# Kernel optimization log

Measured on AMD Instinct MI355X. Metric: run time of the kernel, lower is better.

## Reference

```python
import jax, jax.numpy as jnp
import numpy as np

B, T, I, H, E = 256, 128, 512, 1024, 256


def setup_inputs() -> dict:
    key = jax.random.key(0)
    ks = jax.random.split(key, 14)
    s = lambda *d: 1.0 / np.sqrt(d[-1])
    inp = {
        "x": jax.random.normal(ks[0], (B, T, I), jnp.float32),
        # encoder LSTMCell(I, H): weights [4H, *], gate order i,f,g,o (torch)
        "enc_Wih": jax.random.uniform(ks[1], (4 * H, I), jnp.float32, -s(H), s(H)),
        "enc_Whh": jax.random.uniform(ks[2], (4 * H, H), jnp.float32, -s(H), s(H)),
        "enc_bih": jax.random.uniform(ks[3], (4 * H,), jnp.float32, -s(H), s(H)),
        "enc_bhh": jax.random.uniform(ks[4], (4 * H,), jnp.float32, -s(H), s(H)),
        # enc_fc: H -> E
        "encfc_W": jax.random.uniform(ks[5], (E, H), jnp.float32, -s(H), s(H)),
        "encfc_b": jax.random.uniform(ks[6], (E,), jnp.float32, -s(H), s(H)),
        # dec_fc: E -> H
        "decfc_W": jax.random.uniform(ks[7], (H, E), jnp.float32, -s(E), s(E)),
        "decfc_b": jax.random.uniform(ks[8], (H,), jnp.float32, -s(E), s(E)),
        # decoder LSTMCell(H + I, I)
        "dec_Wih": jax.random.uniform(ks[9], (4 * I, H + I), jnp.float32, -s(I), s(I)),
        "dec_Whh": jax.random.uniform(ks[10], (4 * I, I), jnp.float32, -s(I), s(I)),
        "dec_bih": jax.random.uniform(ks[11], (4 * I,), jnp.float32, -s(I), s(I)),
        "dec_bhh": jax.random.uniform(ks[12], (4 * I,), jnp.float32, -s(I), s(I)),
    }
    return inp


def _gates(pre):
    i, f, g, o = jnp.split(pre, 4, axis=-1)
    return jax.nn.sigmoid(i), jax.nn.sigmoid(f), jnp.tanh(g), jax.nn.sigmoid(o)


def reference(x, enc_Wih, enc_Whh, enc_bih, enc_bhh, encfc_W, encfc_b,
              decfc_W, decfc_b, dec_Wih, dec_Whh, dec_bih, dec_bhh):
    b = x.shape[0]
    # ---- encoder: precompute input projections for all timesteps ----
    x_proj = jnp.einsum('btd,gd->tbg', x, enc_Wih) + (enc_bih + enc_bhh)  # [T,B,4H]

    def enc_step(carry, xp):
        h, c = carry
        i, f, g, o = _gates(xp + h @ enc_Whh.T)
        c = f * c + i * g
        h = o * jnp.tanh(c)
        return (h, c), None

    h0 = jnp.zeros((b, H), x.dtype)
    c0 = jnp.zeros((b, H), x.dtype)
    (_, c_final), _ = jax.lax.scan(enc_step, (h0, c0), x_proj)

    # NB: original code names the returned (h, c) as (o_t_enc, h_t_enc), so
    # embd is computed from the final CELL state -- replicated faithfully.
    embd = jax.nn.relu(c_final @ encfc_W.T + encfc_b)                # [B,E]
    dec_first_hidden = jax.nn.relu(embd @ decfc_W.T + decfc_b)       # [B,H]

    # ---- decoder: input at each step is cat(dec_first_hidden, h_prev) ----
    # (eval path: teacher forcing disabled; dec states init to zeros)
    fixed = dec_first_hidden @ dec_Wih[:, :H].T + (dec_bih + dec_bhh)  # [B,4I]
    W_rec = dec_Wih[:, H:] + dec_Whh  # input second-half and hidden are both h_prev

    def dec_step(carry, _):
        h, c = carry
        i, f, g, o = _gates(fixed + h @ W_rec.T)
        c = f * c + i * g
        h = o * jnp.tanh(c)
        return (h, c), h

    hd0 = jnp.zeros((b, I), x.dtype)
    cd0 = jnp.zeros((b, I), x.dtype)
    _, hs = jax.lax.scan(dec_step, (hd0, cd0), None, length=x.shape[1])  # [T,B,I]
    outputs = jnp.transpose(hs[::-1], (1, 0, 2))  # reversed, [B,T,I]
    return outputs, embd
```

## Files before the change

### kernel.cpp

```cpp
#include <hip/hip_runtime.h>
#include <hip/hip_fp16.h>


#define B_ 256
#define T_ 128
#define I_ 512
#define H_ 1024
#define E_ 256

typedef _Float16 half8 __attribute__((ext_vector_type(8)));
typedef float floatx4 __attribute__((ext_vector_type(4)));

__device__ __forceinline__ float sigmoidf_(float x) { return 1.0f / (1.0f + __expf(-x)); }
__device__ __forceinline__ float tanhf_(float x) {
    x = fminf(fmaxf(x, -15.0f), 15.0f);
    float e = __expf(2.0f * x);
    return (e - 1.0f) / (e + 1.0f);
}

__device__ __forceinline__ half8 ldg_h8_sc1(const _Float16* p) {
    union { unsigned long long u[2]; half8 h; } v;
    const unsigned long long* q = (const unsigned long long*)p;
    v.u[0] = __hip_atomic_load(q,     __ATOMIC_RELAXED, __HIP_MEMORY_SCOPE_AGENT);
    v.u[1] = __hip_atomic_load(q + 1, __ATOMIC_RELAXED, __HIP_MEMORY_SCOPE_AGENT);
    return v.h;
}
__device__ __forceinline__ void stg_h2_sc1(_Float16* p, float a, float b) {
    union { _Float16 h[2]; unsigned int u; } v;
    v.h[0] = (_Float16)a; v.h[1] = (_Float16)b;
    __hip_atomic_store((unsigned int*)p, v.u, __ATOMIC_RELAXED, __HIP_MEMORY_SCOPE_AGENT);
}
__device__ __forceinline__ void wait_vm0() {
    asm volatile("s_waitcnt vmcnt(0)" ::: "memory");
}
__device__ __forceinline__ void poll_rg(int* flags, int rgbase, int lane, int target) {
    while (__hip_atomic_load(&flags[rgbase + lane], __ATOMIC_RELAXED, __HIP_MEMORY_SCOPE_AGENT) < target)
        __builtin_amdgcn_s_sleep(1);
    asm volatile("" ::: "memory");
}

__global__ void shuffle_x_kernel(const float* __restrict__ x, _Float16* __restrict__ xf) {
    const int gg   = blockIdx.x * 256 + threadIdx.x;
    const int tile = gg >> 6;
    const int lane = gg & 63;
    const int t  = tile >> 8;
    const int rt = (tile >> 4) & 15;
    const int kc = tile & 15;
    const int b  = rt * 16 + (lane & 15);
    const int j0 = kc * 32 + ((lane >> 4) << 3);
    const float* src = x + ((size_t)b * T_ + t) * I_ + j0;
    float4 f0 = *(const float4*)src;
    float4 f1 = *(const float4*)(src + 4);
    half8 h = { (_Float16)f0.x, (_Float16)f0.y, (_Float16)f0.z, (_Float16)f0.w,
                (_Float16)f1.x, (_Float16)f1.y, (_Float16)f1.z, (_Float16)f1.w };
    *(half8*)(xf + (size_t)tile * 512 + lane * 8) = h;
}

__global__ __launch_bounds__(256) void small_gemm_kernel(
    const float* __restrict__ A, int lda,
    const float* __restrict__ W, int ldw,
    const float* __restrict__ b1, const float* __restrict__ b2,
    float* __restrict__ out, int N, int K, int relu)
{
    __shared__ float sA2[32][33];
    __shared__ float sW2[32][33];
    int tid = threadIdx.x;
    int tx = tid & 15, ty = tid >> 4;
    int m0 = blockIdx.y * 32, n0 = blockIdx.x * 32;
    float acc[2][2] = {};
    for (int k0 = 0; k0 < K; k0 += 32) {
        __syncthreads();
#pragma unroll
        for (int i = 0; i < 4; ++i) {
            int e = tid + i * 256;
            int r = e >> 5, c = e & 31;
            sA2[r][c] = A[(size_t)(m0 + r) * lda + k0 + c];
            sW2[r][c] = W[(size_t)(n0 + r) * ldw + k0 + c];
        }
        __syncthreads();
#pragma unroll
        for (int k = 0; k < 32; ++k) {
            float a0 = sA2[ty * 2][k], a1 = sA2[ty * 2 + 1][k];
            float w0 = sW2[tx * 2][k], w1 = sW2[tx * 2 + 1][k];
            acc[0][0] += a0 * w0; acc[0][1] += a0 * w1;
            acc[1][0] += a1 * w0; acc[1][1] += a1 * w1;
        }
    }
#pragma unroll
    for (int i = 0; i < 2; ++i)
#pragma unroll
        for (int j = 0; j < 2; ++j) {
            int m = m0 + ty * 2 + i, n = n0 + tx * 2 + j;
            float v = acc[i][j] + b1[n] + (b2 ? b2[n] : 0.0f);
            if (relu) v = fmaxf(v, 0.0f);
            out[(size_t)m * N + n] = v;
        }
}

__global__ __launch_bounds__(256, 1) void enc_persist(
    const _Float16* __restrict__ xf,
    const float* __restrict__ Wih, const float* __restrict__ Whh,
    const float* __restrict__ bih, const float* __restrict__ bhh,
    _Float16* __restrict__ hbuf, float* __restrict__ c_out, int* __restrict__ flags)
{
    const int tid  = threadIdx.x;
    const int wave = tid >> 6, lane = tid & 63;
    const int q = lane >> 4, n15 = lane & 15;
    const int blk = blockIdx.x;
    const int rg = blk >> 6, cc = blk & 63;

    half8 bw[4][12];
#pragma unroll
    for (int g = 0; g < 4; ++g) {
        const int jc = g * H_ + cc * 16 + n15;
#pragma unroll
        for (int kc = 0; kc < 12; ++kc) {
            const int k = (4 * kc + wave) * 32 + q * 8;
            const float* src = (k < I_) ? (Wih + (size_t)jc * I_ + k)
                                        : (Whh + (size_t)jc * H_ + (k - I_));
            float4 f0 = *(const float4*)src;
            float4 f1 = *(const float4*)(src + 4);
            bw[g][kc] = half8{(_Float16)f0.x, (_Float16)f0.y, (_Float16)f0.z, (_Float16)f0.w,
                              (_Float16)f1.x, (_Float16)f1.y, (_Float16)f1.z, (_Float16)f1.w};
        }
    }

    const int hcp = tid & 7;
    const int rT  = tid >> 3;
    float breg[4][2];
#pragma unroll
    for (int g = 0; g < 4; ++g)
#pragma unroll
        for (int e = 0; e < 2; ++e) {
            const int j = g * H_ + cc * 16 + 2 * hcp + e;
            breg[g][e] = bih[j] + bhh[j];
        }
    float creg[2][2] = {{0.f, 0.f}, {0.f, 0.f}};

    __shared__ float preT[4][64][35];
    const size_t laneoff = (size_t)lane * 8;

    for (int s = 0; s < T_; ++s) {
        const _Float16* __restrict__ hcur = hbuf + (size_t)(s & 1) * 262144;
        _Float16* __restrict__ hnxt = hbuf + (size_t)((s + 1) & 1) * 262144;

        floatx4 acc[4][4];
#pragma unroll
        for (int m = 0; m < 4; ++m)
#pragma unroll
            for (int n = 0; n < 4; ++n) acc[m][n] = floatx4{0.f, 0.f, 0.f, 0.f};

        half8 X[4][4];
#pragma unroll
        for (int kc = 0; kc < 4; ++kc)
#pragma unroll
            for (int m = 0; m < 4; ++m)
                X[kc][m] = *(const half8*)(xf + (((size_t)s * 16 + rg * 4 + m) * 16
                                                + (4 * kc + wave)) * 512 + laneoff);
#pragma unroll
        for (int kc = 0; kc < 4; ++kc)
#pragma unroll
            for (int n = 0; n < 4; ++n)
#pragma unroll
                for (int m = 0; m < 4; ++m)
                    acc[m][n] = __builtin_amdgcn_mfma_f32_16x16x32_f16(
                        X[kc][m], bw[n][kc], acc[m][n], 0, 0, 0);

        poll_rg(flags, rg * 64, lane, s);

        half8 Hb[4][4];
#pragma unroll
        for (int kc = 4; kc < 8; ++kc)
#pragma unroll
            for (int m = 0; m < 4; ++m)
                Hb[kc - 4][m] = ldg_h8_sc1(hcur + ((size_t)(rg * 4 + m) * 32
                                                   + (4 * kc + wave - 16)) * 512 + laneoff);
#pragma unroll
        for (int kc = 4; kc < 12; ++kc) {
            const int sl = kc & 3;
#pragma unroll
            for (int n = 0; n < 4; ++n)
#pragma unroll
                for (int m = 0; m < 4; ++m)
                    acc[m][n] = __builtin_amdgcn_mfma_f32_16x16x32_f16(
                        Hb[sl][m], bw[n][kc], acc[m][n], 0, 0, 0);
            if (kc < 8) {
#pragma unroll
                for (int m = 0; m < 4; ++m)
                    Hb[sl][m] = ldg_h8_sc1(hcur + ((size_t)(rg * 4 + m) * 32
                                                   + (4 * (kc + 4) + wave - 16)) * 512 + laneoff);
            }
        }

#pragma unroll
        for (int p = 0; p < 2; ++p) {
            if (p) __syncthreads();
#pragma unroll
            for (int m = 0; m < 2; ++m)
#pragma unroll
                for (int n = 0; n < 4; ++n)
#pragma unroll
                    for (int r = 0; r < 4; ++r)
                        preT[wave][n * 16 + n15][m * 16 + q * 4 + r] = acc[p * 2 + m][n][r];
            __syncthreads();
            float pg[4][2];
#pragma unroll
            for (int g = 0; g < 4; ++g)
#pragma unroll
                for (int e = 0; e < 2; ++e) {
                    const int col = g * 16 + 2 * hcp + e;
                    pg[g][e] = preT[0][col][rT] + preT[1][col][rT]
                             + preT[2][col][rT] + preT[3][col][rT] + breg[g][e];
                }
            float hv[2];
#pragma unroll
            for (int e = 0; e < 2; ++e) {
                const float ig = sigmoidf_(pg[0][e]);
                const float fg = sigmoidf_(pg[1][e]);
                const float gg = tanhf_(pg[2][e]);
                const float og = sigmoidf_(pg[3][e]);
                const float c  = fg * creg[p][e] + ig * gg;
                creg[p][e] = c;
                hv[e] = og * tanhf_(c);
            }
            const int row = p * 32 + rT;
            const int j   = cc * 16 + 2 * hcp;
            const int kch = j >> 5, j5 = j & 31;
            const int lt  = (row & 15) | ((j5 >> 3) << 4);
            stg_h2_sc1(hnxt + ((size_t)(rg * 4 + (row >> 4)) * 32 + kch) * 512
                            + lt * 8 + (j5 & 7), hv[0], hv[1]);
        }

        wait_vm0();
        __syncthreads();
        if (tid == 0)
            __hip_atomic_store(&flags[blk], s + 1, __ATOMIC_RELAXED, __HIP_MEMORY_SCOPE_AGENT);
    }

#pragma unroll
    for (int p = 0; p < 2; ++p)
        *(float2*)(c_out + (size_t)(rg * 64 + p * 32 + rT) * H_ + cc * 16 + 2 * hcp)
            = float2{creg[p][0], creg[p][1]};
}

__global__ __launch_bounds__(256, 1) void dec_persist(
    const float* __restrict__ dWih, const float* __restrict__ dWhh,
    const float* __restrict__ fixedb,
    _Float16* __restrict__ hbuf, float* __restrict__ out, int* __restrict__ flags)
{
    const int tid  = threadIdx.x;
    const int wave = tid >> 6, lane = tid & 63;
    const int q = lane >> 4, n15 = lane & 15;
    const int blk = blockIdx.x;
    const int rg = blk >> 6, cc = blk & 63;

    half8 bw[2][4];
#pragma unroll
    for (int n = 0; n < 2; ++n) {
        const int jc = (n * 2 + (n15 >> 3)) * I_ + cc * 8 + (n15 & 7);
#pragma unroll
        for (int kc = 0; kc < 4; ++kc) {
            const int k = wave * 128 + kc * 32 + q * 8;
            const float* s0 = dWih + (size_t)jc * (H_ + I_) + H_ + k;
            const float* s1 = dWhh + (size_t)jc * I_ + k;
            float4 a0 = *(const float4*)s0, a1 = *(const float4*)(s0 + 4);
            float4 b0 = *(const float4*)s1, b1 = *(const float4*)(s1 + 4);
            bw[n][kc] = half8{(_Float16)(a0.x + b0.x), (_Float16)(a0.y + b0.y),
                              (_Float16)(a0.z + b0.z), (_Float16)(a0.w + b0.w),
                              (_Float16)(a1.x + b1.x), (_Float16)(a1.y + b1.y),
                              (_Float16)(a1.z + b1.z), (_Float16)(a1.w + b1.w)};
        }
    }

    const int hcp = tid & 3;
    const int rT  = tid >> 2;
    const int brow = rg * 64 + rT;
    float fx[4][2];
#pragma unroll
    for (int g = 0; g < 4; ++g)
#pragma unroll
        for (int e = 0; e < 2; ++e)
            fx[g][e] = fixedb[(size_t)brow * (4 * I_) + g * I_ + cc * 8 + 2 * hcp + e];
    float creg2[2] = {0.f, 0.f};

    __shared__ float preT[4][32][67];
    const size_t laneoff = (size_t)lane * 8;

    for (int s = 0; s < T_; ++s) {
        const _Float16* __restrict__ hcur = hbuf + (size_t)(s & 1) * 131072;
        _Float16* __restrict__ hnxt = hbuf + (size_t)((s + 1) & 1) * 131072;

        poll_rg(flags, rg * 64, lane, s);

        half8 Hb[4][4];
#pragma unroll
        for (int kc = 0; kc < 4; ++kc)
#pragma unroll
            for (int m = 0; m < 4; ++m)
                Hb[kc][m] = ldg_h8_sc1(hcur + ((size_t)(rg * 4 + m) * 16
                                               + (wave * 4 + kc)) * 512 + laneoff);
        floatx4 acc[4][2];
#pragma unroll
        for (int m = 0; m < 4; ++m)
#pragma unroll
            for (int n = 0; n < 2; ++n) acc[m][n] = floatx4{0.f, 0.f, 0.f, 0.f};
#pragma unroll
        for (int kc = 0; kc < 4; ++kc)
#pragma unroll
            for (int n = 0; n < 2; ++n)
#pragma unroll
                for (int m = 0; m < 4; ++m)
                    acc[m][n] = __builtin_amdgcn_mfma_f32_16x16x32_f16(
                        Hb[kc][m], bw[n][kc], acc[m][n], 0, 0, 0);

#pragma unroll
        for (int p = 0; p < 2; ++p) {
            if (p) __syncthreads();
#pragma unroll
            for (int m = 0; m < 2; ++m)
#pragma unroll
                for (int n = 0; n < 2; ++n)
#pragma unroll
                    for (int r = 0; r < 4; ++r)
                        preT[wave][n * 16 + n15][m * 16 + q * 4 + r] = acc[p * 2 + m][n][r];
            __syncthreads();
            if ((rT >> 5) == p) {
                const int rl = rT & 31;
                float pg[4][2];
#pragma unroll
                for (int g = 0; g < 4; ++g)
#pragma unroll
                    for (int e = 0; e < 2; ++e) {
                        const int col = (g >> 1) * 16 + (g & 1) * 8 + 2 * hcp + e;
                        pg[g][e] = preT[0][col][rl] + preT[1][col][rl]
                                 + preT[2][col][rl] + preT[3][col][rl] + fx[g][e];
                    }
                float hv[2];
#pragma unroll
                for (int e = 0; e < 2; ++e) {
                    const float ig = sigmoidf_(pg[0][e]);
                    const float fg = sigmoidf_(pg[1][e]);
                    const float gg = tanhf_(pg[2][e]);
                    const float og = sigmoidf_(pg[3][e]);
                    const float c  = fg * creg2[e] + ig * gg;
                    creg2[e] = c;
                    hv[e] = og * tanhf_(c);
                }
                *(float2*)(out + ((size_t)brow * T_ + (T_ - 1 - s)) * I_ + cc * 8 + 2 * hcp)
                    = float2{hv[0], hv[1]};
                const int j = cc * 8 + 2 * hcp;
                const int kch = j >> 5, j5 = j & 31;
                const int lt  = (rT & 15) | ((j5 >> 3) << 4);
                stg_h2_sc1(hnxt + ((size_t)(rg * 4 + (rT >> 4)) * 16 + kch) * 512
                                + lt * 8 + (j5 & 7), hv[0], hv[1]);
            }
        }

        wait_vm0();
        __syncthreads();
        if (tid == 0)
            __hip_atomic_store(&flags[blk], s + 1, __ATOMIC_RELAXED, __HIP_MEMORY_SCOPE_AGENT);
    }
}

extern "C" void kernel_launch(void* const* d_in, const int* in_sizes, int n_in,
                              void* d_out_v, int out_size, void* d_ws, size_t ws_size,
                              hipStream_t stream) {
    (void)in_sizes; (void)n_in; (void)out_size; (void)ws_size;
    const float* x    = (const float*)d_in[0];
    const float* eWih = (const float*)d_in[1];
    const float* eWhh = (const float*)d_in[2];
    const float* ebih = (const float*)d_in[3];
    const float* ebhh = (const float*)d_in[4];
    const float* efcW = (const float*)d_in[5];
    const float* efcb = (const float*)d_in[6];
    const float* dfcW = (const float*)d_in[7];
    const float* dfcb = (const float*)d_in[8];
    const float* dWih = (const float*)d_in[9];
    const float* dWhh = (const float*)d_in[10];
    const float* dbih = (const float*)d_in[11];
    const float* dbhh = (const float*)d_in[12];
    float* d_out = (float*)d_out_v;

    char* ws = (char*)d_ws;
    size_t off = 0;
    auto carve = [&](size_t bytes) {
        char* p = ws + off;
        off += (bytes + 255) & ~(size_t)255;
        return p;
    };
    _Float16* xf     = (_Float16*)carve((size_t)B_ * T_ * I_ * 2);
    _Float16* hbufE  = (_Float16*)carve((size_t)2 * 262144 * 2);
    _Float16* hbufD  = (_Float16*)carve((size_t)2 * 131072 * 2);
    float*    c_e    = (float*)carve((size_t)B_ * H_ * 4);
    float*    fixedb = (float*)carve((size_t)B_ * 4 * I_ * 4);
    float*    dec1   = (float*)carve((size_t)B_ * H_ * 4);
    int*      flagsE = (int*)carve(256 * 4);
    int*      flagsD = (int*)carve(256 * 4);

    hipMemsetAsync(flagsE, 0, 256 * 4, stream);
    hipMemsetAsync(flagsD, 0, 256 * 4, stream);
    hipMemsetAsync(hbufE, 0, (size_t)262144 * 2, stream);
    hipMemsetAsync(hbufD, 0, (size_t)131072 * 2, stream);

    shuffle_x_kernel<<<dim3(8192), 256, 0, stream>>>(x, xf);

    enc_persist<<<dim3(256), 256, 0, stream>>>(xf, eWih, eWhh, ebih, ebhh,
                                               hbufE, c_e, flagsE);

    float* embd = d_out + (size_t)B_ * T_ * I_;
    small_gemm_kernel<<<dim3(E_ / 32, B_ / 32), 256, 0, stream>>>(
        c_e, H_, efcW, H_, efcb, nullptr, embd, E_, H_, 1);
    small_gemm_kernel<<<dim3(H_ / 32, B_ / 32), 256, 0, stream>>>(
        embd, E_, dfcW, E_, dfcb, nullptr, dec1, H_, E_, 1);
    small_gemm_kernel<<<dim3(4 * I_ / 32, B_ / 32), 256, 0, stream>>>(
        dec1, H_, dWih, H_ + I_, dbih, dbhh, fixedb, 4 * I_, H_, 0);

    dec_persist<<<dim3(256), 256, 0, stream>>>(dWih, dWhh, fixedb,
                                               hbufD, d_out, flagsD);
}
```

Baseline: 1.851 ms.

## Replace flag-based step sync with sentinel-filled per-step hidden buffers

The encoder and decoder persistent kernels no longer publish per-block step flags or poll them before loading the previous hidden state. Each timestep now writes to its own slice of a buffer sized T+1 steps, pre-filled with a 0x7C sentinel pattern. Consumers spin until the loaded chunks contain no sentinel words. This removes the flag round trip and the vmcnt(0) drain before signalling, so the next step can start as soon as its data lands. The cost is a much larger workspace and large memsets per call, and it relies on the fp16 sentinel (two +inf halves per word) never occurring in real data. The old flag path is kept as a fallback when the workspace is too small.

```diff
diff --git a/kernel.cpp b/kernel.cpp
--- a/kernel.cpp
+++ b/kernel.cpp
@@ -8,6 +8,10 @@
 #define H_ 1024
 #define E_ 256
 
+#define ENC_STEP 262144
+#define DEC_STEP 131072
+#define SENT32 0x7C7C7C7Cu
+
 typedef _Float16 half8 __attribute__((ext_vector_type(8)));
 typedef float floatx4 __attribute__((ext_vector_type(4)));
 
@@ -18,12 +22,33 @@
     return (e - 1.0f) / (e + 1.0f);
 }
 
-__device__ __forceinline__ half8 ldg_h8_sc1(const _Float16* p) {
-    union { unsigned long long u[2]; half8 h; } v;
+union HU { unsigned long long u[2]; half8 h; };
+
+__device__ __forceinline__ void ld_chunk(const _Float16* p, HU& v) {
     const unsigned long long* q = (const unsigned long long*)p;
     v.u[0] = __hip_atomic_load(q,     __ATOMIC_RELAXED, __HIP_MEMORY_SCOPE_AGENT);
     v.u[1] = __hip_atomic_load(q + 1, __ATOMIC_RELAXED, __HIP_MEMORY_SCOPE_AGENT);
-    return v.h;
+}
+__device__ __forceinline__ int chunk_ok(const HU& v) {
+    unsigned a = (unsigned)v.u[0], b = (unsigned)(v.u[0] >> 32);
+    unsigned c = (unsigned)v.u[1], d = (unsigned)(v.u[1] >> 32);
+    return (int)((a != SENT32) & (b != SENT32) & (c != SENT32) & (d != SENT32));
+}
+template <int STRIDE>
+__device__ __forceinline__ void load_grp(const _Float16* base, HU v[4]) {
+#pragma unroll
+    for (int m = 0; m < 4; ++m) ld_chunk(base + (size_t)m * STRIDE, v[m]);
+}
+template <int STRIDE>
+__device__ __forceinline__ void fix_grp(const _Float16* base, HU v[4]) {
+    while (!(chunk_ok(v[0]) & chunk_ok(v[1]) & chunk_ok(v[2]) & chunk_ok(v[3]))) {
+        __builtin_amdgcn_s_sleep(1);
+        load_grp<STRIDE>(base, v);
+    }
+}
+
+__device__ __forceinline__ half8 ldg_h8_sc1(const _Float16* p) {
+    HU v; ld_chunk(p, v); return v.h;
 }
 __device__ __forceinline__ void stg_h2_sc1(_Float16* p, float a, float b) {
     union { _Float16 h[2]; unsigned int u; } v;
@@ -97,11 +122,11 @@
         }
 }
 
-__global__ __launch_bounds__(256, 1) void enc_persist(
+__global__ __launch_bounds__(256, 1) void enc_df(
     const _Float16* __restrict__ xf,
     const float* __restrict__ Wih, const float* __restrict__ Whh,
     const float* __restrict__ bih, const float* __restrict__ bhh,
-    _Float16* __restrict__ hbuf, float* __restrict__ c_out, int* __restrict__ flags)
+    _Float16* __restrict__ hbuf, float* __restrict__ c_out)
 {
     const int tid  = threadIdx.x;
     const int wave = tid >> 6, lane = tid & 63;
@@ -141,8 +166,8 @@
     const size_t laneoff = (size_t)lane * 8;
 
     for (int s = 0; s < T_; ++s) {
-        const _Float16* __restrict__ hcur = hbuf + (size_t)(s & 1) * 262144;
-        _Float16* __restrict__ hnxt = hbuf + (size_t)((s + 1) & 1) * 262144;
+        const _Float16* __restrict__ hcur = hbuf + (size_t)s * ENC_STEP;
+        _Float16* __restrict__ hnxt = hbuf + (size_t)(s + 1) * ENC_STEP;
 
         floatx4 acc[4][4];
 #pragma unroll
@@ -166,30 +191,25 @@
                     acc[m][n] = __builtin_amdgcn_mfma_f32_16x16x32_f16(
                         X[kc][m], bw[n][kc], acc[m][n], 0, 0, 0);
 
-        poll_rg(flags, rg * 64, lane, s);
-
-        half8 Hb[4][4];
+        HU Hb[4][4];
 #pragma unroll
         for (int kc = 4; kc < 8; ++kc)
-#pragma unroll
-            for (int m = 0; m < 4; ++m)
-                Hb[kc - 4][m] = ldg_h8_sc1(hcur + ((size_t)(rg * 4 + m) * 32
-                                                   + (4 * kc + wave - 16)) * 512 + laneoff);
+            load_grp<32 * 512>(hcur + ((size_t)(rg * 4) * 32 + (4 * kc + wave - 16)) * 512
+                                    + laneoff, Hb[kc - 4]);
 #pragma unroll
         for (int kc = 4; kc < 12; ++kc) {
             const int sl = kc & 3;
+            fix_grp<32 * 512>(hcur + ((size_t)(rg * 4) * 32 + (4 * kc + wave - 16)) * 512
+                                   + laneoff, Hb[sl]);
 #pragma unroll
             for (int n = 0; n < 4; ++n)
 #pragma unroll
                 for (int m = 0; m < 4; ++m)
                     acc[m][n] = __builtin_amdgcn_mfma_f32_16x16x32_f16(
-                        Hb[sl][m], bw[n][kc], acc[m][n], 0, 0, 0);
-            if (kc < 8) {
-#pragma unroll
-                for (int m = 0; m < 4; ++m)
-                    Hb[sl][m] = ldg_h8_sc1(hcur + ((size_t)(rg * 4 + m) * 32
-                                                   + (4 * (kc + 4) + wave - 16)) * 512 + laneoff);
-            }
+                        Hb[sl][m].h, bw[n][kc], acc[m][n], 0, 0, 0);
+            if (kc < 8)
+                load_grp<32 * 512>(hcur + ((size_t)(rg * 4) * 32 + (4 * (kc + 4) + wave - 16)) * 512
+                                        + laneoff, Hb[sl]);
         }
 
 #pragma unroll
@@ -230,11 +250,7 @@
             stg_h2_sc1(hnxt + ((size_t)(rg * 4 + (row >> 4)) * 32 + kch) * 512
                             + lt * 8 + (j5 & 7), hv[0], hv[1]);
         }
-
-        wait_vm0();
         __syncthreads();
-        if (tid == 0)
-            __hip_atomic_store(&flags[blk], s + 1, __ATOMIC_RELAXED, __HIP_MEMORY_SCOPE_AGENT);
     }
 
 #pragma unroll
@@ -243,10 +259,10 @@
             = float2{creg[p][0], creg[p][1]};
 }
 
-__global__ __launch_bounds__(256, 1) void dec_persist(
+__global__ __launch_bounds__(256, 1) void dec_df(
     const float* __restrict__ dWih, const float* __restrict__ dWhh,
     const float* __restrict__ fixedb,
-    _Float16* __restrict__ hbuf, float* __restrict__ out, int* __restrict__ flags)
+    _Float16* __restrict__ hbuf, float* __restrict__ out)
 {
     const int tid  = threadIdx.x;
     const int wave = tid >> 6, lane = tid & 63;
@@ -287,31 +303,31 @@
     const size_t laneoff = (size_t)lane * 8;
 
     for (int s = 0; s < T_; ++s) {
-        const _Float16* __restrict__ hcur = hbuf + (size_t)(s & 1) * 131072;
-        _Float16* __restrict__ hnxt = hbuf + (size_t)((s + 1) & 1) * 131072;
-
-        poll_rg(flags, rg * 64, lane, s);
-
-        half8 Hb[4][4];
+        const _Float16* __restrict__ hcur = hbuf + (size_t)s * DEC_STEP;
+        _Float16* __restrict__ hnxt = hbuf + (size_t)(s + 1) * DEC_STEP;
+
+        HU Hb[4][4];
 #pragma unroll
         for (int kc = 0; kc < 4; ++kc)
-#pragma unroll
-            for (int m = 0; m < 4; ++m)
-                Hb[kc][m] = ldg_h8_sc1(hcur + ((size_t)(rg * 4 + m) * 16
-                                               + (wave * 4 + kc)) * 512 + laneoff);
+            load_grp<16 * 512>(hcur + ((size_t)(rg * 4) * 16 + (wave * 4 + kc)) * 512
+                                    + laneoff, Hb[kc]);
+
         floatx4 acc[4][2];
 #pragma unroll
         for (int m = 0; m < 4; ++m)
 #pragma unroll
             for (int n = 0; n < 2; ++n) acc[m][n] = floatx4{0.f, 0.f, 0.f, 0.f};
 #pragma unroll
-        for (int kc = 0; kc < 4; ++kc)
+        for (int kc = 0; kc < 4; ++kc) {
+            fix_grp<16 * 512>(hcur + ((size_t)(rg * 4) * 16 + (wave * 4 + kc)) * 512
+                                   + laneoff, Hb[kc]);
 #pragma unroll
             for (int n = 0; n < 2; ++n)
 #pragma unroll
                 for (int m = 0; m < 4; ++m)
                     acc[m][n] = __builtin_amdgcn_mfma_f32_16x16x32_f16(
-                        Hb[kc][m], bw[n][kc], acc[m][n], 0, 0, 0);
+                        Hb[kc][m].h, bw[n][kc], acc[m][n], 0, 0, 0);
+        }
 
 #pragma unroll
         for (int p = 0; p < 2; ++p) {
@@ -355,18 +371,280 @@
                                 + lt * 8 + (j5 & 7), hv[0], hv[1]);
             }
         }
+        __syncthreads();
+    }
+}
+
+__global__ __launch_bounds__(256, 1) void enc_persist(
+    const _Float16* __restrict__ xf,
+    const float* __restrict__ Wih, const float* __restrict__ Whh,
+    const float* __restrict__ bih, const float* __restrict__ bhh,
+    _Float16* __restrict__ hbuf, float* __restrict__ c_out, int* __restrict__ flags)
+{
+    const int tid  = threadIdx.x;
+    const int wave = tid >> 6, lane = tid & 63;
+    const int q = lane >> 4, n15 = lane & 15;
+    const int blk = blockIdx.x;
+    const int rg = blk >> 6, cc = blk & 63;
+
+    half8 bw[4][12];
+#pragma unroll
+    for (int g = 0; g < 4; ++g) {
+        const int jc = g * H_ + cc * 16 + n15;
+#pragma unroll
+        for (int kc = 0; kc < 12; ++kc) {
+            const int k = (4 * kc + wave) * 32 + q * 8;
+            const float* src = (k < I_) ? (Wih + (size_t)jc * I_ + k)
+                                        : (Whh + (size_t)jc * H_ + (k - I_));
+            float4 f0 = *(const float4*)src;
+            float4 f1 = *(const float4*)(src + 4);
+            bw[g][kc] = half8{(_Float16)f0.x, (_Float16)f0.y, (_Float16)f0.z, (_Float16)f0.w,
+                              (_Float16)f1.x, (_Float16)f1.y, (_Float16)f1.z, (_Float16)f1.w};
+        }
+    }
+
+    const int hcp = tid & 7;
+    const int rT  = tid >> 3;
+    float breg[4][2];
+#pragma unroll
+    for (int g = 0; g < 4; ++g)
+#pragma unroll
+        for (int e = 0; e < 2; ++e) {
+            const int j = g * H_ + cc * 16 + 2 * hcp + e;
+            breg[g][e] = bih[j] + bhh[j];
+        }
+    float creg[2][2] = {{0.f, 0.f}, {0.f, 0.f}};
+
+    __shared__ float preT[4][64][35];
+    const size_t laneoff = (size_t)lane * 8;
+
+    for (int s = 0; s < T_; ++s) {
+        const _Float16* __restrict__ hcur = hbuf + (size_t)(s & 1) * 262144;
+        _Float16* __restrict__ hnxt = hbuf + (size_t)((s + 1) & 1) * 262144;
+
+        floatx4 acc[4][4];
+#pragma unroll
+        for (int m = 0; m < 4; ++m)
+#pragma unroll
+            for (int n = 0; n < 4; ++n) acc[m][n] = floatx4{0.f, 0.f, 0.f, 0.f};
+
+        half8 X[4][4];
+#pragma unroll
+        for (int kc = 0; kc < 4; ++kc)
+#pragma unroll
+            for (int m = 0; m < 4; ++m)
+                X[kc][m] = *(const half8*)(xf + (((size_t)s * 16 + rg * 4 + m) * 16
+                                                + (4 * kc + wave)) * 512 + laneoff);
+#pragma unroll
+        for (int kc = 0; kc < 4; ++kc)
+#pragma unroll
+            for (int n = 0; n < 4; ++n)
+#pragma unroll
+                for (int m = 0; m < 4; ++m)
+                    acc[m][n] = __builtin_amdgcn_mfma_f32_16x16x32_f16(
+                        X[kc][m], bw[n][kc], acc[m][n], 0, 0, 0);
+
+        poll_rg(flags, rg * 64, lane, s);
+
+        half8 Hb[4][4];
+#pragma unroll
+        for (int kc = 4; kc < 8; ++kc)
+#pragma unroll
+            for (int m = 0; m < 4; ++m)
+                Hb[kc - 4][m] = ldg_h8_sc1(hcur + ((size_t)(rg * 4 + m) * 32
+                                                   + (4 * kc + wave - 16)) * 512 + laneoff);
+#pragma unroll
+        for (int kc = 4; kc < 12; ++kc) {
+            const int sl = kc & 3;
+#pragma unroll
+            for (int n = 0; n < 4; ++n)
+#pragma unroll
+                for (int m = 0; m < 4; ++m)
+                    acc[m][n] = __builtin_amdgcn_mfma_f32_16x16x32_f16(
+                        Hb[sl][m], bw[n][kc], acc[m][n], 0, 0, 0);
+            if (kc < 8) {
+#pragma unroll
+                for (int m = 0; m < 4; ++m)
+                    Hb[sl][m] = ldg_h8_sc1(hcur + ((size_t)(rg * 4 + m) * 32
+                                                   + (4 * (kc + 4) + wave - 16)) * 512 + laneoff);
+            }
+        }
+
+#pragma unroll
+        for (int p = 0; p < 2; ++p) {
+            if (p) __syncthreads();
+#pragma unroll
+            for (int m = 0; m < 2; ++m)
+#pragma unroll
+                for (int n = 0; n < 4; ++n)
+#pragma unroll
+                    for (int r = 0; r < 4; ++r)
+                        preT[wave][n * 16 + n15][m * 16 + q * 4 + r] = acc[p * 2 + m][n][r];
+            __syncthreads();
+            float pg[4][2];
+#pragma unroll
+            for (int g = 0; g < 4; ++g)
+#pragma unroll
+                for (int e = 0; e < 2; ++e) {
+                    const int col = g * 16 + 2 * hcp + e;
+                    pg[g][e] = preT[0][col][rT] + preT[1][col][rT]
+                             + preT[2][col][rT] + preT[3][col][rT] + breg[g][e];
+                }
+            float hv[2];
+#pragma unroll
+            for (int e = 0; e < 2; ++e) {
+                const float ig = sigmoidf_(pg[0][e]);
+                const float fg = sigmoidf_(pg[1][e]);
+                const float gg = tanhf_(pg[2][e]);
+                const float og = sigmoidf_(pg[3][e]);
+                const float c  = fg * creg[p][e] + ig * gg;
+                creg[p][e] = c;
+                hv[e] = og * tanhf_(c);
+            }
+            const int row = p * 32 + rT;
+            const int j   = cc * 16 + 2 * hcp;
+            const int kch = j >> 5, j5 = j & 31;
+            const int lt  = (row & 15) | ((j5 >> 3) << 4);
+            stg_h2_sc1(hnxt + ((size_t)(rg * 4 + (row >> 4)) * 32 + kch) * 512
+                            + lt * 8 + (j5 & 7), hv[0], hv[1]);
+        }
 
         wait_vm0();
         __syncthreads();
         if (tid == 0)
             __hip_atomic_store(&flags[blk], s + 1, __ATOMIC_RELAXED, __HIP_MEMORY_SCOPE_AGENT);
     }
+
+#pragma unroll
+    for (int p = 0; p < 2; ++p)
+        *(float2*)(c_out + (size_t)(rg * 64 + p * 32 + rT) * H_ + cc * 16 + 2 * hcp)
+            = float2{creg[p][0], creg[p][1]};
+}
+
+__global__ __launch_bounds__(256, 1) void dec_persist(
+    const float* __restrict__ dWih, const float* __restrict__ dWhh,
+    const float* __restrict__ fixedb,
+    _Float16* __restrict__ hbuf, float* __restrict__ out, int* __restrict__ flags)
+{
+    const int tid  = threadIdx.x;
+    const int wave = tid >> 6, lane = tid & 63;
+    const int q = lane >> 4, n15 = lane & 15;
+    const int blk = blockIdx.x;
+    const int rg = blk >> 6, cc = blk & 63;
+
+    half8 bw[2][4];
+#pragma unroll
+    for (int n = 0; n < 2; ++n) {
+        const int jc = (n * 2 + (n15 >> 3)) * I_ + cc * 8 + (n15 & 7);
+#pragma unroll
+        for (int kc = 0; kc < 4; ++kc) {
+            const int k = wave * 128 + kc * 32 + q * 8;
+            const float* s0 = dWih + (size_t)jc * (H_ + I_) + H_ + k;
+            const float* s1 = dWhh + (size_t)jc * I_ + k;
+            float4 a0 = *(const float4*)s0, a1 = *(const float4*)(s0 + 4);
+            float4 b0 = *(const float4*)s1, b1 = *(const float4*)(s1 + 4);
+            bw[n][kc] = half8{(_Float16)(a0.x + b0.x), (_Float16)(a0.y + b0.y),
+                              (_Float16)(a0.z + b0.z), (_Float16)(a0.w + b0.w),
+                              (_Float16)(a1.x + b1.x), (_Float16)(a1.y + b1.y),
+                              (_Float16)(a1.z + b1.z), (_Float16)(a1.w + b1.w)};
+        }
+    }
+
+    const int hcp = tid & 3;
+    const int rT  = tid >> 2;
+    const int brow = rg * 64 + rT;
+    float fx[4][2];
+#pragma unroll
+    for (int g = 0; g < 4; ++g)
+#pragma unroll
+        for (int e = 0; e < 2; ++e)
+            fx[g][e] = fixedb[(size_t)brow * (4 * I_) + g * I_ + cc * 8 + 2 * hcp + e];
+    float creg2[2] = {0.f, 0.f};
+
+    __shared__ float preT[4][32][67];
+    const size_t laneoff = (size_t)lane * 8;
+
+    for (int s = 0; s < T_; ++s) {
+        const _Float16* __restrict__ hcur = hbuf + (size_t)(s & 1) * 131072;
+        _Float16* __restrict__ hnxt = hbuf + (size_t)((s + 1) & 1) * 131072;
+
+        poll_rg(flags, rg * 64, lane, s);
+
+        half8 Hb[4][4];
+#pragma unroll
+        for (int kc = 0; kc < 4; ++kc)
+#pragma unroll
+            for (int m = 0; m < 4; ++m)
+                Hb[kc][m] = ldg_h8_sc1(hcur + ((size_t)(rg * 4 + m) * 16
+                                               + (wave * 4 + kc)) * 512 + laneoff);
+        floatx4 acc[4][2];
+#pragma unroll
+        for (int m = 0; m < 4; ++m)
+#pragma unroll
+            for (int n = 0; n < 2; ++n) acc[m][n] = floatx4{0.f, 0.f, 0.f, 0.f};
+#pragma unroll
+        for (int kc = 0; kc < 4; ++kc)
+#pragma unroll
+            for (int n = 0; n < 2; ++n)
+#pragma unroll
+                for (int m = 0; m < 4; ++m)
+                    acc[m][n] = __builtin_amdgcn_mfma_f32_16x16x32_f16(
+                        Hb[kc][m], bw[n][kc], acc[m][n], 0, 0, 0);
+
+#pragma unroll
+        for (int p = 0; p < 2; ++p) {
+            if (p) __syncthreads();
+#pragma unroll
+            for (int m = 0; m < 2; ++m)
+#pragma unroll
+                for (int n = 0; n < 2; ++n)
+#pragma unroll
+                    for (int r = 0; r < 4; ++r)
+                        preT[wave][n * 16 + n15][m * 16 + q * 4 + r] = acc[p * 2 + m][n][r];
+            __syncthreads();
+            if ((rT >> 5) == p) {
+                const int rl = rT & 31;
+                float pg[4][2];
+#pragma unroll
+                for (int g = 0; g < 4; ++g)
+#pragma unroll
+                    for (int e = 0; e < 2; ++e) {
+                        const int col = (g >> 1) * 16 + (g & 1) * 8 + 2 * hcp + e;
+                        pg[g][e] = preT[0][col][rl] + preT[1][col][rl]
+                                 + preT[2][col][rl] + preT[3][col][rl] + fx[g][e];
+                    }
+                float hv[2];
+#pragma unroll
+                for (int e = 0; e < 2; ++e) {
+                    const float ig = sigmoidf_(pg[0][e]);
+                    const float fg = sigmoidf_(pg[1][e]);
+                    const float gg = tanhf_(pg[2][e]);
+                    const float og = sigmoidf_(pg[3][e]);
+                    const float c  = fg * creg2[e] + ig * gg;
+                    creg2[e] = c;
+                    hv[e] = og * tanhf_(c);
+                }
+                *(float2*)(out + ((size_t)brow * T_ + (T_ - 1 - s)) * I_ + cc * 8 + 2 * hcp)
+                    = float2{hv[0], hv[1]};
+                const int j = cc * 8 + 2 * hcp;
+                const int kch = j >> 5, j5 = j & 31;
+                const int lt  = (rT & 15) | ((j5 >> 3) << 4);
+                stg_h2_sc1(hnxt + ((size_t)(rg * 4 + (rT >> 4)) * 16 + kch) * 512
+                                + lt * 8 + (j5 & 7), hv[0], hv[1]);
+            }
+        }
+
+        wait_vm0();
+        __syncthreads();
+        if (tid == 0)
+            __hip_atomic_store(&flags[blk], s + 1, __ATOMIC_RELAXED, __HIP_MEMORY_SCOPE_AGENT);
+    }
 }
 
 extern "C" void kernel_launch(void* const* d_in, const int* in_sizes, int n_in,
                               void* d_out_v, int out_size, void* d_ws, size_t ws_size,
                               hipStream_t stream) {
-    (void)in_sizes; (void)n_in; (void)out_size; (void)ws_size;
+    (void)in_sizes; (void)n_in; (void)out_size;
     const float* x    = (const float*)d_in[0];
     const float* eWih = (const float*)d_in[1];
     const float* eWhh = (const float*)d_in[2];
@@ -389,33 +667,65 @@
         off += (bytes + 255) & ~(size_t)255;
         return p;
     };
-    _Float16* xf     = (_Float16*)carve((size_t)B_ * T_ * I_ * 2);
-    _Float16* hbufE  = (_Float16*)carve((size_t)2 * 262144 * 2);
-    _Float16* hbufD  = (_Float16*)carve((size_t)2 * 131072 * 2);
-    float*    c_e    = (float*)carve((size_t)B_ * H_ * 4);
-    float*    fixedb = (float*)carve((size_t)B_ * 4 * I_ * 4);
-    float*    dec1   = (float*)carve((size_t)B_ * H_ * 4);
-    int*      flagsE = (int*)carve(256 * 4);
-    int*      flagsD = (int*)carve(256 * 4);
-
-    hipMemsetAsync(flagsE, 0, 256 * 4, stream);
-    hipMemsetAsync(flagsD, 0, 256 * 4, stream);
-    hipMemsetAsync(hbufE, 0, (size_t)262144 * 2, stream);
-    hipMemsetAsync(hbufD, 0, (size_t)131072 * 2, stream);
-
-    shuffle_x_kernel<<<dim3(8192), 256, 0, stream>>>(x, xf);
-
-    enc_persist<<<dim3(256), 256, 0, stream>>>(xf, eWih, eWhh, ebih, ebhh,
-                                               hbufE, c_e, flagsE);
+
+    const size_t xf_b  = (size_t)B_ * T_ * I_ * 2;
+    const size_t hbE_b = (size_t)(T_ + 1) * ENC_STEP * 2;
+    const size_t hbD_b = (size_t)(T_ + 1) * DEC_STEP * 2;
+    const size_t ce_b  = (size_t)B_ * H_ * 4;
+    const size_t fxb_b = (size_t)B_ * 4 * I_ * 4;
+    const size_t d1_b  = (size_t)B_ * H_ * 4;
+    const size_t need_primary = xf_b + hbE_b + hbD_b + ce_b + fxb_b + d1_b + 4096;
 
     float* embd = d_out + (size_t)B_ * T_ * I_;
-    small_gemm_kernel<<<dim3(E_ / 32, B_ / 32), 256, 0, stream>>>(
-        c_e, H_, efcW, H_, efcb, nullptr, embd, E_, H_, 1);
-    small_gemm_kernel<<<dim3(H_ / 32, B_ / 32), 256, 0, stream>>>(
-        embd, E_, dfcW, E_, dfcb, nullptr, dec1, H_, E_, 1);
-    small_gemm_kernel<<<dim3(4 * I_ / 32, B_ / 32), 256, 0, stream>>>(
-        dec1, H_, dWih, H_ + I_, dbih, dbhh, fixedb, 4 * I_, H_, 0);
-
-    dec_persist<<<dim3(256), 256, 0, stream>>>(dWih, dWhh, fixedb,
-                                               hbufD, d_out, flagsD);
-}
+
+    if (ws_size == 0 || ws_size >= need_primary) {
+        _Float16* xf     = (_Float16*)carve(xf_b);
+        _Float16* hbufE  = (_Float16*)carve(hbE_b);
+        _Float16* hbufD  = (_Float16*)carve(hbD_b);
+        float*    c_e    = (float*)carve(ce_b);
+        float*    fixedb = (float*)carve(fxb_b);
+        float*    dec1   = (float*)carve(d1_b);
+
+        hipMemsetAsync(hbufE, 0, (size_t)ENC_STEP * 2, stream);
+        hipMemsetAsync((char*)hbufE + (size_t)ENC_STEP * 2, 0x7C, (size_t)T_ * ENC_STEP * 2, stream);
+        hipMemsetAsync(hbufD, 0, (size_t)DEC_STEP * 2, stream);
+        hipMemsetAsync((char*)hbufD + (size_t)DEC_STEP * 2, 0x7C, (size_t)T_ * DEC_STEP * 2, stream);
+
+        shuffle_x_kernel<<<dim3(8192), 256, 0, stream>>>(x, xf);
+        enc_df<<<dim3(256), 256, 0, stream>>>(xf, eWih, eWhh, ebih, ebhh, hbufE, c_e);
+        small_gemm_kernel<<<dim3(E_ / 32, B_ / 32), 256, 0, stream>>>(
+            c_e, H_, efcW, H_, efcb, nullptr, embd, E_, H_, 1);
+        small_gemm_kernel<<<dim3(H_ / 32, B_ / 32), 256, 0, stream>>>(
+            embd, E_, dfcW, E_, dfcb, nullptr, dec1, H_, E_, 1);
+        small_gemm_kernel<<<dim3(4 * I_ / 32, B_ / 32), 256, 0, stream>>>(
+            dec1, H_, dWih, H_ + I_, dbih, dbhh, fixedb, 4 * I_, H_, 0);
+        dec_persist;
+        dec_df<<<dim3(256), 256, 0, stream>>>(dWih, dWhh, fixedb, hbufD, d_out);
+    } else {
+        _Float16* xf     = (_Float16*)carve(xf_b);
+        _Float16* hbufE  = (_Float16*)carve((size_t)2 * 262144 * 2);
+        _Float16* hbufD  = (_Float16*)carve((size_t)2 * 131072 * 2);
+        float*    c_e    = (float*)carve(ce_b);
+        float*    fixedb = (float*)carve(fxb_b);
+        float*    dec1   = (float*)carve(d1_b);
+        int*      flagsE = (int*)carve(256 * 4);
+        int*      flagsD = (int*)carve(256 * 4);
+
+        hipMemsetAsync(flagsE, 0, 256 * 4, stream);
+        hipMemsetAsync(flagsD, 0, 256 * 4, stream);
+        hipMemsetAsync(hbufE, 0, (size_t)262144 * 2, stream);
+        hipMemsetAsync(hbufD, 0, (size_t)131072 * 2, stream);
+
+        shuffle_x_kernel<<<dim3(8192), 256, 0, stream>>>(x, xf);
+        enc_persist<<<dim3(256), 256, 0, stream>>>(xf, eWih, eWhh, ebih, ebhh,
+                                                   hbufE, c_e, flagsE);
+        small_gemm_kernel<<<dim3(E_ / 32, B_ / 32), 256, 0, stream>>>(
+            c_e, H_, efcW, H_, efcb, nullptr, embd, E_, H_, 1);
+        small_gemm_kernel<<<dim3(H_ / 32, B_ / 32), 256, 0, stream>>>(
+            embd, E_, dfcW, E_, dfcb, nullptr, dec1, H_, E_, 1);
+        small_gemm_kernel<<<dim3(4 * I_ / 32, B_ / 32), 256, 0, stream>>>(
+            dec1, H_, dWih, H_ + I_, dbih, dbhh, fixedb, 4 * I_, H_, 0);
+        dec_persist<<<dim3(256), 256, 0, stream>>>(dWih, dWhh, fixedb,
+                                                   hbufD, d_out, flagsD);
+    }
+}
```

Measured after the change: 1.779 ms. 1.04x faster.
